# Kernel optimization log

Hardware: AMD Instinct MI355X
Metric: run time of the kernel (lower is better)

## Reference

```python
import jax, jax.numpy as jnp
import numpy as np

GROUPS = 32
EPS = 1e-5


def setup_inputs() -> dict:
    key = jax.random.key(0)
    ks = jax.random.split(key, 7)
    B, C, H, W = 32, 512, 32, 32
    x = jax.random.normal(ks[0], (B, C, H, W), dtype=jnp.float32)
    # GroupNorm affine params
    gn_w = jnp.ones((C,), dtype=jnp.float32)
    gn_b = jnp.zeros((C,), dtype=jnp.float32)
    # 1x1 Conv1d == matmul over channel dim
    qkv_w = jax.random.normal(ks[1], (3 * C, C), dtype=jnp.float32) * (C ** -0.5)
    qkv_b = jax.random.normal(ks[2], (3 * C,), dtype=jnp.float32) * 0.02
    proj_w = jax.random.normal(ks[3], (C, C), dtype=jnp.float32) * (C ** -0.5)
    proj_b = jax.random.normal(ks[4], (C,), dtype=jnp.float32) * 0.02
    return {"x": x, "gn_w": gn_w, "gn_b": gn_b, "qkv_w": qkv_w,
            "qkv_b": qkv_b, "proj_w": proj_w, "proj_b": proj_b}


def _group_norm(x, w, b):
    B, C, H, W = x.shape
    xg = x.reshape(B, GROUPS, C // GROUPS, H, W)
    mean = xg.mean(axis=(2, 3, 4), keepdims=True)
    var = xg.var(axis=(2, 3, 4), keepdims=True)
    xg = (xg - mean) * jax.lax.rsqrt(var + EPS)
    return xg.reshape(B, C, H, W) * w[None, :, None, None] + b[None, :, None, None]


def reference(x, gn_w, gn_b, qkv_w, qkv_b, proj_w, proj_b):
    B, C, H, W = x.shape
    h = _group_norm(x, gn_w, gn_b).reshape(B, C, H * W)  # [B, C, N]
    qkv = jnp.einsum('oc,bcn->bon', qkv_w, h) + qkv_b[None, :, None]  # [B, 3C, N]
    q, k, v = jnp.split(qkv, 3, axis=1)
    scale = C ** (-0.5)
    # scores: q^T k  -> [B, N, N]
    attn = jax.nn.softmax(jnp.einsum('bcn,bcm->bnm', q, k) * scale, axis=-1)
    # h = v @ attn^T -> [B, C, N]
    h = jnp.einsum('bcm,bnm->bcn', v, attn)
    h = jnp.einsum('oc,bcn->bon', proj_w, h) + proj_b[None, :, None]
    return x + h.reshape(B, C, H, W)
```

## Files before the change

kernel.cpp:

```cpp
#include <hip/hip_runtime.h>
#include <stdint.h>

typedef __bf16 bf16;
typedef __bf16 bf16x4 __attribute__((ext_vector_type(4)));
typedef __bf16 bf16x8 __attribute__((ext_vector_type(8)));
typedef float f32x4 __attribute__((ext_vector_type(4)));

#define CN 524288
#define NPIX 1024
#define CCH 512

__device__ __forceinline__ void gload_lds16(const void* g, void* l) {
  auto gp = reinterpret_cast<const __attribute__((address_space(1))) uint32_t*>(
      reinterpret_cast<uintptr_t>(g));
  auto lp = reinterpret_cast<__attribute__((address_space(3))) uint32_t*>(
      static_cast<uint32_t>(reinterpret_cast<uintptr_t>(l)));
  __builtin_amdgcn_global_load_lds(gp, lp, 16, 0, 0);
}

template<int EPI>
__global__ __launch_bounds__(512, 2)
void gemm_bt(const bf16* __restrict__ A, int lda, long long sA,
             const bf16* __restrict__ Bt, int ldb, long long sB,
             char* __restrict__ Cp, long long sC,
             char* __restrict__ C2p, long long sC2,
             const float* __restrict__ bias,
             const float* __restrict__ resid,
             float* __restrict__ pst,
             int K, float scale)
{
  __shared__ __align__(16) bf16 As[2 * 16384];
  __shared__ __align__(16) bf16 Bs[2 * 16384];
  const int t = threadIdx.x;
  const int w = t >> 6;
  const int l = t & 63;
  const int z = blockIdx.z;
  A  += (long long)z * sA;
  Bt += (long long)z * sB;
  Cp += (long long)z * sC;
  if (C2p) C2p += (long long)z * sC2;
  const float* residb = (EPI == 3) ? (resid + (long long)z * CN) : nullptr;

  const int row0 = blockIdx.x * 256;
  const int col0 = blockIdx.y * 256;
  const int wr = w >> 2;
  const int wc = w & 3;

  f32x4 acc[8][4] = {};

  const int wv  = w;
  const int srow = (l >> 3);
  const int segp = ((l & 7) ^ srow) << 3;
  const bf16* baseA = A  + (long long)(row0 + wv * 8 + srow) * lda + segp;
  const bf16* baseB = Bt + (long long)(col0 + wv * 8 + srow) * ldb + segp;

  auto stageA = [&](int kt1, int buf, int c) {
    gload_lds16(baseA + (long long)c * 64 * lda + kt1 * 64,
                &As[buf * 16384 + c * 4096 + wv * 512]);
  };
  auto stageB = [&](int kt1, int buf, int c) {
    gload_lds16(baseB + (long long)c * 64 * ldb + kt1 * 64,
                &Bs[buf * 16384 + c * 4096 + wv * 512]);
  };

  const int lrow = l & 15;
  const int lx = l & 7;
  const int s0 = (((l >> 4)) ^ lx) << 3;
  const int s1 = (((l >> 4) + 4) ^ lx) << 3;

  const int nt = K >> 6;

  #pragma unroll
  for (int c = 0; c < 4; ++c) stageB(0, 0, c);
  #pragma unroll
  for (int c = 0; c < 4; ++c) stageA(0, 0, c);

  #pragma unroll 1
  for (int kt = 0; kt < nt; ++kt) {
    const int cur = kt & 1, nxt = cur ^ 1;
    const bool pf = (kt + 1) < nt;
    if (pf) {
      #pragma unroll
      for (int c = 0; c < 4; ++c) stageB(kt + 1, nxt, c);
      asm volatile("s_waitcnt vmcnt(4)" ::: "memory");
    } else {
      asm volatile("s_waitcnt vmcnt(0)" ::: "memory");
    }
    __builtin_amdgcn_sched_barrier(0);
    __builtin_amdgcn_s_barrier();
    asm volatile("" ::: "memory");

    const int ca = cur * 16384;
    bf16x8 bF0[4], bF1[4], aF0[4], aF1[4];
    #pragma unroll
    for (int nf = 0; nf < 4; ++nf) {
      const int r = wc * 64 + nf * 16 + lrow;
      bF0[nf] = *(const bf16x8*)&Bs[ca + r * 64 + s0];
      bF1[nf] = *(const bf16x8*)&Bs[ca + r * 64 + s1];
    }
    #pragma unroll
    for (int mf = 0; mf < 4; ++mf) {
      const int r = wr * 128 + mf * 16 + lrow;
      aF0[mf] = *(const bf16x8*)&As[ca + r * 64 + s0];
      aF1[mf] = *(const bf16x8*)&As[ca + r * 64 + s1];
    }
    __builtin_amdgcn_s_setprio(1);
    #pragma unroll
    for (int mf = 0; mf < 4; ++mf)
      #pragma unroll
      for (int nf = 0; nf < 4; ++nf)
        acc[mf][nf] = __builtin_amdgcn_mfma_f32_16x16x32_bf16(
            aF1[mf], bF1[nf],
            __builtin_amdgcn_mfma_f32_16x16x32_bf16(aF0[mf], bF0[nf], acc[mf][nf], 0, 0, 0),
            0, 0, 0);
    __builtin_amdgcn_s_setprio(0);
    if (pf) {
      #pragma unroll
      for (int c = 0; c < 4; ++c) stageA(kt + 1, nxt, c);
    }
    #pragma unroll
    for (int mf = 0; mf < 4; ++mf) {
      const int r = wr * 128 + 64 + mf * 16 + lrow;
      aF0[mf] = *(const bf16x8*)&As[ca + r * 64 + s0];
      aF1[mf] = *(const bf16x8*)&As[ca + r * 64 + s1];
    }
    __builtin_amdgcn_s_setprio(1);
    #pragma unroll
    for (int mf = 0; mf < 4; ++mf)
      #pragma unroll
      for (int nf = 0; nf < 4; ++nf)
        acc[4 + mf][nf] = __builtin_amdgcn_mfma_f32_16x16x32_bf16(
            aF1[mf], bF1[nf],
            __builtin_amdgcn_mfma_f32_16x16x32_bf16(aF0[mf], bF0[nf], acc[4 + mf][nf], 0, 0, 0),
            0, 0, 0);
    __builtin_amdgcn_s_setprio(0);
    asm volatile("" ::: "memory");
    __builtin_amdgcn_sched_barrier(0);
    __builtin_amdgcn_s_barrier();
  }

  const int ci = (l >> 4) * 4;
  const int cj = l & 15;

  if constexpr (EPI == 1) {
    bf16* sp = (bf16*)Cp;
    float* part = (float*)As;
    #pragma unroll
    for (int mf = 0; mf < 8; ++mf) {
      const int lr0 = wr * 128 + mf * 16 + ci;
      #pragma unroll
      for (int r = 0; r < 4; ++r) {
        float s = 0.f;
        #pragma unroll
        for (int nf = 0; nf < 4; ++nf) {
          const int j = col0 + wc * 64 + nf * 16 + cj;
          const float u = __expf(acc[mf][nf][r] * scale);
          const bf16 ub = (bf16)u;
          sp[(row0 + lr0 + r) * NPIX + j] = ub;
          s += (float)ub;
        }
        s += __shfl_xor(s, 1); s += __shfl_xor(s, 2);
        s += __shfl_xor(s, 4); s += __shfl_xor(s, 8);
        if (cj == 0) part[wc * 256 + lr0 + r] = s;
      }
    }
    __syncthreads();
    if (t < 256)
      pst[((long long)z * 4 + blockIdx.y) * 1024 + row0 + t]
          = part[t] + part[256 + t] + part[512 + t] + part[768 + t];
    return;
  }

  #pragma unroll
  for (int mf = 0; mf < 8; ++mf) {
    const int i0 = row0 + wr * 128 + mf * 16 + ci;
    if constexpr (EPI == 2) {
      const float* pz = pst + (long long)z * 4096;
      #pragma unroll
      for (int r = 0; r < 4; ++r) {
        const int row = i0 + r;
        const float is = 1.f / (pz[row] + pz[1024 + row] +
                                pz[2048 + row] + pz[3072 + row]);
        bf16* hp = (bf16*)Cp;
        #pragma unroll
        for (int nf = 0; nf < 4; ++nf) {
          const int j = col0 + wc * 64 + nf * 16 + cj;
          hp[row * CCH + j] = (bf16)(acc[mf][nf][r] * is);
        }
      }
    } else {
      #pragma unroll
      for (int nf = 0; nf < 4; ++nf) {
        const int j = col0 + wc * 64 + nf * 16 + cj;
        const f32x4 a = acc[mf][nf];
        if constexpr (EPI == 0) {
          const float bj = bias[j];
          if (j < NPIX) {
            bf16* q = (bf16*)Cp;
            #pragma unroll
            for (int r = 0; r < 4; ++r)
              q[(i0 + r) * NPIX + j] = (bf16)(a[r] + bj);
          } else {
            bf16* vb = (bf16*)C2p;
            #pragma unroll
            for (int r = 0; r < 4; ++r)
              vb[(j - NPIX) * NPIX + (i0 + r)] = (bf16)(a[r] + bj);
          }
        } else {
          float* op = (float*)Cp;
          #pragma unroll
          for (int r = 0; r < 4; ++r)
            op[(i0 + r) * NPIX + j] = a[r] + bias[i0 + r] + residb[(i0 + r) * NPIX + j];
        }
      }
    }
  }
}

__global__ __launch_bounds__(256)
void gn_fused(const float* __restrict__ x, const float* __restrict__ gw,
              const float* __restrict__ gb, bf16* __restrict__ hnT)
{
  __shared__ float xs[16 * 1024];
  __shared__ float red[8];
  const int b = blockIdx.x >> 5;
  const int g = blockIdx.x & 31;
  const float* xp = x + ((long long)b * CCH + g * 16) * NPIX;
  const int t = threadIdx.x;

  float4* xsv = (float4*)xs;
  const float4* gv = (const float4*)xp;
  float s = 0.f, ss = 0.f;
  #pragma unroll
  for (int i = 0; i < 16; ++i) {
    float4 v = gv[t + i * 256];
    xsv[t + i * 256] = v;
    s  += v.x + v.y + v.z + v.w;
    ss += v.x * v.x + v.y * v.y + v.z * v.z + v.w * v.w;
  }
  #pragma unroll
  for (int o = 32; o; o >>= 1) { s += __shfl_xor(s, o); ss += __shfl_xor(ss, o); }
  if ((t & 63) == 0) { red[t >> 6] = s; red[4 + (t >> 6)] = ss; }
  __syncthreads();
  s  = red[0] + red[1] + red[2] + red[3];
  ss = red[4] + red[5] + red[6] + red[7];
  const float mean = s * (1.f / 16384.f);
  const float var  = ss * (1.f / 16384.f) - mean * mean;
  const float rstd = rsqrtf(var + 1e-5f);

  float ac[16], bc[16];
  #pragma unroll
  for (int c = 0; c < 16; ++c) {
    const float wv = gw[g * 16 + c] * rstd;
    ac[c] = wv;
    bc[c] = gb[g * 16 + c] - mean * wv;
  }

  bf16* hp = hnT + (long long)b * CN + g * 16;
  #pragma unroll
  for (int r = 0; r < 4; ++r) {
    const int n = t + r * 256;
    bf16x8 o0, o1;
    #pragma unroll
    for (int c = 0; c < 8; ++c)
      o0[c] = (bf16)(xs[c * 1024 + n] * ac[c] + bc[c]);
    #pragma unroll
    for (int c = 0; c < 8; ++c)
      o1[c] = (bf16)(xs[(8 + c) * 1024 + n] * ac[8 + c] + bc[8 + c]);
    *(bf16x8*)&hp[(long long)n * CCH]     = o0;
    *(bf16x8*)&hp[(long long)n * CCH + 8] = o1;
  }
}

__global__ __launch_bounds__(256)
void cvt_weights(const float* __restrict__ qw, const float* __restrict__ pw,
                 bf16* __restrict__ qwb, bf16* __restrict__ pwb)
{
  const int i = blockIdx.x * 256 + threadIdx.x;
  if (i < 3 * CCH * CCH) qwb[i] = (bf16)qw[i];
  if (i < CCH * CCH) pwb[i] = (bf16)pw[i];
}

extern "C" void kernel_launch(void* const* d_in, const int* in_sizes, int n_in,
                              void* d_out, int out_size, void* d_ws, size_t ws_size,
                              hipStream_t stream)
{
  const float* x      = (const float*)d_in[0];
  const float* gn_w   = (const float*)d_in[1];
  const float* gn_b   = (const float*)d_in[2];
  const float* qkv_w  = (const float*)d_in[3];
  const float* qkv_b  = (const float*)d_in[4];
  const float* proj_w = (const float*)d_in[5];
  const float* proj_b = (const float*)d_in[6];
  float* out = (float*)d_out;
  (void)in_sizes; (void)n_in; (void)out_size;

  char* ws = (char*)d_ws;
  size_t off = 0;
  auto alloc = [&](size_t bytes) -> char* {
    char* p = ws + off;
    off += (bytes + 255) & ~(size_t)255;
    return p;
  };
  bf16* qkv_wb  = (bf16*)alloc(3 * 512 * 512 * 2);
  bf16* proj_wb = (bf16*)alloc(512 * 512 * 2);
  const size_t fixed = off;
  const size_t per = 1048576ull + 2097152ull + 1048576ull + 2097152ull
                   + 1048576ull + 16384ull;
  int Bc = 32;
  if (ws_size > fixed) {
    size_t fit = (ws_size - fixed) / per;
    if (fit < 32) Bc = (int)fit;
  } else {
    Bc = 0;
  }
  if (Bc < 1) Bc = 1;

  bf16*  hnT    = (bf16*) alloc((size_t)Bc * 1048576);
  bf16*  qkT    = (bf16*) alloc((size_t)Bc * 2097152);
  bf16*  vbuf   = (bf16*) alloc((size_t)Bc * 1048576);
  bf16*  ubuf   = (bf16*) alloc((size_t)Bc * 2097152);
  bf16*  hvT    = (bf16*) alloc((size_t)Bc * 1048576);
  float* pstats = (float*)alloc((size_t)Bc * 16384);

  cvt_weights<<<dim3(3072), 256, 0, stream>>>(qkv_w, proj_w, qkv_wb, proj_wb);

  const float scale = 0.044194173824159216f;
  for (int b0 = 0; b0 < 32; b0 += Bc) {
    const int bc = (32 - b0 < Bc) ? (32 - b0) : Bc;
    const float* xb = x + (size_t)b0 * CN;

    gn_fused<<<dim3(bc * 32), 256, 0, stream>>>(xb, gn_w, gn_b, hnT);

    gemm_bt<0><<<dim3(4, 6, bc), 512, 0, stream>>>(
        hnT, 512, 524288, qkv_wb, 512, 0,
        (char*)qkT, 2097152, (char*)vbuf, 1048576, qkv_b, nullptr, nullptr,
        512, 1.f);

    gemm_bt<1><<<dim3(4, 4, bc), 512, 0, stream>>>(
        qkT, 1024, 1048576, qkT + 512, 1024, 1048576,
        (char*)ubuf, 2097152, nullptr, 0, nullptr, nullptr, pstats,
        512, scale);

    gemm_bt<2><<<dim3(4, 2, bc), 512, 0, stream>>>(
        ubuf, 1024, 1048576, vbuf, 1024, 524288,
        (char*)hvT, 1048576, nullptr, 0, nullptr, nullptr, pstats,
        1024, 1.f);

    gemm_bt<3><<<dim3(2, 4, bc), 512, 0, stream>>>(
        proj_wb, 512, 0, hvT, 512, 524288,
        (char*)(out + (size_t)b0 * CN), 2097152, nullptr, 0, proj_b, xb,
        nullptr, 512, 1.f);
  }
}
```

Baseline: 245.1 us.

## Fold Q and K projections into a single Wq^T Wk matrix for scores

```diff
diff --git a/kernel.cpp b/kernel.cpp
--- a/kernel.cpp
+++ b/kernel.cpp
@@ -40,6 +40,7 @@
   Cp += (long long)z * sC;
   if (C2p) C2p += (long long)z * sC2;
   const float* residb = (EPI == 3) ? (resid + (long long)z * CN) : nullptr;
+  const float* cpartb = (EPI == 1) ? (resid + (long long)z * 32768) : nullptr;
 
   const int row0 = blockIdx.x * 256;
   const int col0 = blockIdx.y * 256;
@@ -143,6 +144,15 @@
   const int cj = l & 15;
 
   if constexpr (EPI == 1) {
+    float cs[4];
+    #pragma unroll
+    for (int nf = 0; nf < 4; ++nf) {
+      const int j = col0 + wc * 64 + nf * 16 + cj;
+      float s = 0.f;
+      #pragma unroll
+      for (int g = 0; g < 32; ++g) s += cpartb[g * 1024 + j];
+      cs[nf] = s;
+    }
     bf16* sp = (bf16*)Cp;
     float* part = (float*)As;
     #pragma unroll
@@ -154,7 +164,7 @@
         #pragma unroll
         for (int nf = 0; nf < 4; ++nf) {
           const int j = col0 + wc * 64 + nf * 16 + cj;
-          const float u = __expf(acc[mf][nf][r] * scale);
+          const float u = __expf((acc[mf][nf][r] + cs[nf]) * scale);
           const bf16 ub = (bf16)u;
           sp[(row0 + lr0 + r) * NPIX + j] = ub;
           s += (float)ub;
@@ -194,18 +204,23 @@
         const int j = col0 + wc * 64 + nf * 16 + cj;
         const f32x4 a = acc[mf][nf];
         if constexpr (EPI == 0) {
-          const float bj = bias[j];
-          if (j < NPIX) {
+          if (j < 512) {
             bf16* q = (bf16*)Cp;
             #pragma unroll
             for (int r = 0; r < 4; ++r)
-              q[(i0 + r) * NPIX + j] = (bf16)(a[r] + bj);
+              q[(i0 + r) * CCH + j] = (bf16)a[r];
           } else {
+            const float bj = bias[512 + j];
             bf16* vb = (bf16*)C2p;
             #pragma unroll
             for (int r = 0; r < 4; ++r)
-              vb[(j - NPIX) * NPIX + (i0 + r)] = (bf16)(a[r] + bj);
+              vb[(j - 512) * NPIX + (i0 + r)] = (bf16)(a[r] + bj);
           }
+        } else if constexpr (EPI == 4) {
+          bf16* gp = (bf16*)Cp;
+          #pragma unroll
+          for (int r = 0; r < 4; ++r)
+            gp[(i0 + r) * CCH + j] = (bf16)a[r];
         } else {
           float* op = (float*)Cp;
           #pragma unroll
@@ -219,7 +234,8 @@
 
 __global__ __launch_bounds__(256)
 void gn_fused(const float* __restrict__ x, const float* __restrict__ gw,
-              const float* __restrict__ gb, bf16* __restrict__ hnT)
+              const float* __restrict__ gb, const float* __restrict__ u,
+              bf16* __restrict__ hnT, float* __restrict__ cpart)
 {
   __shared__ float xs[16 * 1024];
   __shared__ float red[8];
@@ -248,37 +264,87 @@
   const float var  = ss * (1.f / 16384.f) - mean * mean;
   const float rstd = rsqrtf(var + 1e-5f);
 
-  float ac[16], bc[16];
+  float ac[16], bc[16], uu[16];
   #pragma unroll
   for (int c = 0; c < 16; ++c) {
     const float wv = gw[g * 16 + c] * rstd;
     ac[c] = wv;
     bc[c] = gb[g * 16 + c] - mean * wv;
+    uu[c] = u[g * 16 + c];
   }
 
   bf16* hp = hnT + (long long)b * CN + g * 16;
+  float* cp = cpart + ((long long)b * 32 + g) * 1024;
   #pragma unroll
   for (int r = 0; r < 4; ++r) {
     const int n = t + r * 256;
     bf16x8 o0, o1;
-    #pragma unroll
-    for (int c = 0; c < 8; ++c)
-      o0[c] = (bf16)(xs[c * 1024 + n] * ac[c] + bc[c]);
-    #pragma unroll
-    for (int c = 0; c < 8; ++c)
-      o1[c] = (bf16)(xs[(8 + c) * 1024 + n] * ac[8 + c] + bc[8 + c]);
+    float cacc = 0.f;
+    #pragma unroll
+    for (int c = 0; c < 8; ++c) {
+      const float v0 = xs[c * 1024 + n] * ac[c] + bc[c];
+      o0[c] = (bf16)v0;
+      cacc += v0 * uu[c];
+    }
+    #pragma unroll
+    for (int c = 0; c < 8; ++c) {
+      const float v1 = xs[(8 + c) * 1024 + n] * ac[8 + c] + bc[8 + c];
+      o1[c] = (bf16)v1;
+      cacc += v1 * uu[8 + c];
+    }
     *(bf16x8*)&hp[(long long)n * CCH]     = o0;
     *(bf16x8*)&hp[(long long)n * CCH + 8] = o1;
-  }
+    cp[n] = cacc;
+  }
+}
+
+__global__ __launch_bounds__(256)
+void transp2(const float* __restrict__ qkv_w,
+             bf16* __restrict__ qwT, bf16* __restrict__ kwT)
+{
+  __shared__ float tile[32][33];
+  const int zz = blockIdx.z;
+  const float* in = qkv_w + (long long)zz * 512 * 512;
+  bf16* outp = zz ? kwT : qwT;
+  const int r0 = blockIdx.x * 32, c0 = blockIdx.y * 32;
+  const int tx = threadIdx.x, ty = threadIdx.y;
+  #pragma unroll
+  for (int r = 0; r < 32; r += 8)
+    tile[ty + r][tx] = in[(r0 + ty + r) * 512 + c0 + tx];
+  __syncthreads();
+  #pragma unroll
+  for (int r = 0; r < 32; r += 8)
+    outp[(c0 + ty + r) * 512 + r0 + tx] = (bf16)tile[tx][ty + r];
+}
+
+__global__ __launch_bounds__(256)
+void ucalc(const float* __restrict__ qkv_w, const float* __restrict__ qkv_b,
+           float* __restrict__ u)
+{
+  __shared__ float red[4][64];
+  const int d0 = blockIdx.x * 64;
+  const int td = threadIdx.x & 63;
+  const int tg = threadIdx.x >> 6;
+  const float* wk = qkv_w + (long long)512 * 512;
+  float s = 0.f;
+  #pragma unroll 8
+  for (int o = tg * 128; o < tg * 128 + 128; ++o)
+    s += qkv_b[o] * wk[(long long)o * 512 + d0 + td];
+  red[tg][td] = s;
+  __syncthreads();
+  if (threadIdx.x < 64)
+    u[d0 + td] = red[0][td] + red[1][td] + red[2][td] + red[3][td];
 }
 
 __global__ __launch_bounds__(256)
 void cvt_weights(const float* __restrict__ qw, const float* __restrict__ pw,
-                 bf16* __restrict__ qwb, bf16* __restrict__ pwb)
+                 bf16* __restrict__ w2v, bf16* __restrict__ pwb)
 {
   const int i = blockIdx.x * 256 + threadIdx.x;
-  if (i < 3 * CCH * CCH) qwb[i] = (bf16)qw[i];
-  if (i < CCH * CCH) pwb[i] = (bf16)pw[i];
+  if (i < CCH * CCH) {
+    w2v[i] = (bf16)qw[1024 * 512 + i];
+    pwb[i] = (bf16)pw[i];
+  }
 }
 
 extern "C" void kernel_launch(void* const* d_in, const int* in_sizes, int n_in,
@@ -302,11 +368,14 @@
     off += (bytes + 255) & ~(size_t)255;
     return p;
   };
-  bf16* qkv_wb  = (bf16*)alloc(3 * 512 * 512 * 2);
-  bf16* proj_wb = (bf16*)alloc(512 * 512 * 2);
+  bf16*  W2      = (bf16*)alloc(1024 * 512 * 2);
+  bf16*  proj_wb = (bf16*)alloc(512 * 512 * 2);
+  bf16*  qwT     = (bf16*)alloc(512 * 512 * 2);
+  bf16*  kwT     = (bf16*)alloc(512 * 512 * 2);
+  float* uvec    = (float*)alloc(512 * 4);
   const size_t fixed = off;
-  const size_t per = 1048576ull + 2097152ull + 1048576ull + 2097152ull
-                   + 1048576ull + 16384ull;
+  const size_t per = 1048576ull + 1048576ull + 1048576ull + 2097152ull
+                   + 1048576ull + 16384ull + 131072ull;
   int Bc = 32;
   if (ws_size > fixed) {
     size_t fit = (ws_size - fixed) / per;
@@ -317,29 +386,35 @@
   if (Bc < 1) Bc = 1;
 
   bf16*  hnT    = (bf16*) alloc((size_t)Bc * 1048576);
-  bf16*  qkT    = (bf16*) alloc((size_t)Bc * 2097152);
+  bf16*  kgT    = (bf16*) alloc((size_t)Bc * 1048576);
   bf16*  vbuf   = (bf16*) alloc((size_t)Bc * 1048576);
   bf16*  ubuf   = (bf16*) alloc((size_t)Bc * 2097152);
   bf16*  hvT    = (bf16*) alloc((size_t)Bc * 1048576);
   float* pstats = (float*)alloc((size_t)Bc * 16384);
-
-  cvt_weights<<<dim3(3072), 256, 0, stream>>>(qkv_w, proj_w, qkv_wb, proj_wb);
+  float* cpart  = (float*)alloc((size_t)Bc * 131072);
+
+  transp2<<<dim3(16, 16, 2), dim3(32, 8), 0, stream>>>(qkv_w, qwT, kwT);
+  ucalc<<<dim3(8), 256, 0, stream>>>(qkv_w, qkv_b, uvec);
+  cvt_weights<<<dim3(1024), 256, 0, stream>>>(qkv_w, proj_w, W2 + 512 * 512, proj_wb);
+  gemm_bt<4><<<dim3(2, 2, 1), 512, 0, stream>>>(
+      qwT, 512, 0, kwT, 512, 0,
+      (char*)W2, 0, nullptr, 0, nullptr, nullptr, nullptr, 512, 1.f);
 
   const float scale = 0.044194173824159216f;
   for (int b0 = 0; b0 < 32; b0 += Bc) {
     const int bc = (32 - b0 < Bc) ? (32 - b0) : Bc;
     const float* xb = x + (size_t)b0 * CN;
 
-    gn_fused<<<dim3(bc * 32), 256, 0, stream>>>(xb, gn_w, gn_b, hnT);
-
-    gemm_bt<0><<<dim3(4, 6, bc), 512, 0, stream>>>(
-        hnT, 512, 524288, qkv_wb, 512, 0,
-        (char*)qkT, 2097152, (char*)vbuf, 1048576, qkv_b, nullptr, nullptr,
+    gn_fused<<<dim3(bc * 32), 256, 0, stream>>>(xb, gn_w, gn_b, uvec, hnT, cpart);
+
+    gemm_bt<0><<<dim3(4, 4, bc), 512, 0, stream>>>(
+        hnT, 512, 524288, W2, 512, 0,
+        (char*)kgT, 1048576, (char*)vbuf, 1048576, qkv_b, nullptr, nullptr,
         512, 1.f);
 
     gemm_bt<1><<<dim3(4, 4, bc), 512, 0, stream>>>(
-        qkT, 1024, 1048576, qkT + 512, 1024, 1048576,
-        (char*)ubuf, 2097152, nullptr, 0, nullptr, nullptr, pstats,
+        hnT, 512, 524288, kgT, 512, 524288,
+        (char*)ubuf, 2097152, nullptr, 0, nullptr, cpart, pstats,
         512, scale);
 
     gemm_bt<2><<<dim3(4, 2, bc), 512, 0, stream>>>(
```

After: 260.2 us. +6.1%, slower.

## Remap workgroup IDs across XCDs and alias intermediate buffers to shrink workspace

Applied to the files above, without the earlier changes.

```diff
diff --git a/kernel.cpp b/kernel.cpp
--- a/kernel.cpp
+++ b/kernel.cpp
@@ -34,15 +34,23 @@
   const int t = threadIdx.x;
   const int w = t >> 6;
   const int l = t & 63;
-  const int z = blockIdx.z;
+
+  const int gx = gridDim.x, gy = gridDim.y;
+  const int nwg = gx * gy * gridDim.z;
+  int lin = blockIdx.x + gx * (blockIdx.y + gy * blockIdx.z);
+  lin = (lin & 7) * (nwg >> 3) + (lin >> 3);
+  const int bx = lin % gx;
+  const int by = (lin / gx) % gy;
+  const int z  = lin / (gx * gy);
+
   A  += (long long)z * sA;
   Bt += (long long)z * sB;
   Cp += (long long)z * sC;
   if (C2p) C2p += (long long)z * sC2;
   const float* residb = (EPI == 3) ? (resid + (long long)z * CN) : nullptr;
 
-  const int row0 = blockIdx.x * 256;
-  const int col0 = blockIdx.y * 256;
+  const int row0 = bx * 256;
+  const int col0 = by * 256;
   const int wr = w >> 2;
   const int wc = w & 3;
 
@@ -166,7 +174,7 @@
     }
     __syncthreads();
     if (t < 256)
-      pst[((long long)z * 4 + blockIdx.y) * 1024 + row0 + t]
+      pst[((long long)z * 4 + by) * 1024 + row0 + t]
           = part[t] + part[256 + t] + part[512 + t] + part[768 + t];
     return;
   }
@@ -256,7 +264,8 @@
     bc[c] = gb[g * 16 + c] - mean * wv;
   }
 
-  bf16* hp = hnT + (long long)b * CN + g * 16;
+  bf16* hp = hnT + (long long)b * 1048576;
+  hp += g * 16;
   #pragma unroll
   for (int r = 0; r < 4; ++r) {
     const int n = t + r * 256;
@@ -305,8 +314,7 @@
   bf16* qkv_wb  = (bf16*)alloc(3 * 512 * 512 * 2);
   bf16* proj_wb = (bf16*)alloc(512 * 512 * 2);
   const size_t fixed = off;
-  const size_t per = 1048576ull + 2097152ull + 1048576ull + 2097152ull
-                   + 1048576ull + 16384ull;
+  const size_t per = 2097152ull + 2097152ull + 1048576ull + 16384ull;
   int Bc = 32;
   if (ws_size > fixed) {
     size_t fit = (ws_size - fixed) / per;
@@ -316,12 +324,14 @@
   }
   if (Bc < 1) Bc = 1;
 
-  bf16*  hnT    = (bf16*) alloc((size_t)Bc * 1048576);
-  bf16*  qkT    = (bf16*) alloc((size_t)Bc * 2097152);
+  char* regA = alloc((size_t)Bc * 2097152);
+  char* regB = alloc((size_t)Bc * 2097152);
   bf16*  vbuf   = (bf16*) alloc((size_t)Bc * 1048576);
-  bf16*  ubuf   = (bf16*) alloc((size_t)Bc * 2097152);
-  bf16*  hvT    = (bf16*) alloc((size_t)Bc * 1048576);
   float* pstats = (float*)alloc((size_t)Bc * 16384);
+  bf16* hnT  = (bf16*)regA;
+  bf16* ubuf = (bf16*)regA;
+  bf16* qkT  = (bf16*)regB;
+  bf16* hvT  = (bf16*)regB;
 
   cvt_weights<<<dim3(3072), 256, 0, stream>>>(qkv_w, proj_w, qkv_wb, proj_wb);
 
@@ -333,7 +343,7 @@
     gn_fused<<<dim3(bc * 32), 256, 0, stream>>>(xb, gn_w, gn_b, hnT);
 
     gemm_bt<0><<<dim3(4, 6, bc), 512, 0, stream>>>(
-        hnT, 512, 524288, qkv_wb, 512, 0,
+        hnT, 512, 1048576, qkv_wb, 512, 0,
         (char*)qkT, 2097152, (char*)vbuf, 1048576, qkv_b, nullptr, nullptr,
         512, 1.f);
 
@@ -344,11 +354,11 @@
 
     gemm_bt<2><<<dim3(4, 2, bc), 512, 0, stream>>>(
         ubuf, 1024, 1048576, vbuf, 1024, 524288,
-        (char*)hvT, 1048576, nullptr, 0, nullptr, nullptr, pstats,
+        (char*)hvT, 2097152, nullptr, 0, nullptr, nullptr, pstats,
         1024, 1.f);
 
     gemm_bt<3><<<dim3(2, 4, bc), 512, 0, stream>>>(
-        proj_wb, 512, 0, hvT, 512, 524288,
+        proj_wb, 512, 0, hvT, 512, 1048576,
         (char*)(out + (size_t)b0 * CN), 2097152, nullptr, 0, proj_b, xb,
         nullptr, 512, 1.f);
   }
```

Result: faster. 231.5 us (-5.6%).
